# Kernel optimization log

Hardware: AMD Instinct MI355X
Metric: run time of the kernel (lower is better)

Reference implementation:

```python
import jax, jax.numpy as jnp
from jax import lax
import numpy as np

EPS = 1e-5  # BatchNorm eps


def setup_inputs() -> dict:
    key = jax.random.key(0)
    ks = jax.random.split(key, 4)
    T, B, C = 256, 128, 1024
    L, H, NCLS = 6, 1024, 1000
    x = jax.random.normal(ks[0], (T, B, C), dtype=jnp.float32)
    W = jax.random.normal(ks[1], (L, C, H), dtype=jnp.float32) * (1.0 / np.sqrt(C))
    b = jnp.zeros((L, H), dtype=jnp.float32)
    gamma = jnp.ones((L, H), dtype=jnp.float32)
    beta = jnp.zeros((L, H), dtype=jnp.float32)
    u = jax.random.uniform(ks[2], (L, H), dtype=jnp.float32)  # recurrent weights in (0, U_bound~1)
    Wc = jax.random.normal(ks[3], (H, NCLS), dtype=jnp.float32) * (1.0 / np.sqrt(H))
    bc = jnp.zeros((NCLS,), dtype=jnp.float32)
    return {"x": x, "W": W, "b": b, "gamma": gamma, "beta": beta, "u": u, "Wc": Wc, "bc": bc}


def _layer(h, Wl, bl, gl, betal, ul):
    # per-timestep dense projection: [T,B,Cin] @ [Cin,H]
    z = jnp.einsum('tbi,ih->tbh', h, Wl) + bl
    # BN over (time, batch) per channel (bn_before, training-mode batch stats)
    mean = jnp.mean(z, axis=(0, 1))
    var = jnp.var(z, axis=(0, 1))
    z = (z - mean) * (gl / jnp.sqrt(var + EPS)) + betal
    # IndRNN diagonal recurrence: h_t = relu(z_t + u * h_{t-1}), h_0 = 0
    T, B, H = z.shape
    def step(hprev, zt):
        hnew = jax.nn.relu(zt + ul * hprev)
        return hnew, hnew
    _, hs = lax.scan(step, jnp.zeros((B, H), dtype=z.dtype), z)
    return hs


def reference(x, W, b, gamma, beta, u, Wc, bc):
    h = x
    for l in range(W.shape[0]):
        h = _layer(h, W[l], b[l], gamma[l], beta[l], u[l])
    # classifier on last timestep
    return h[-1] @ Wc + bc
```

## Files before the change

kernel.cpp:

```cpp
#include <hip/hip_runtime.h>
#include <hip/hip_bf16.h>

#define T_DIM 256
#define B_DIM 128
#define C_DIM 1024
#define H_DIM 1024
#define L_DIM 6
#define NC_DIM 1000
#define M_DIM (T_DIM * B_DIM)
#define BH_DIM (B_DIM * H_DIM)

typedef __attribute__((ext_vector_type(8))) short bf16x8;
typedef __attribute__((ext_vector_type(4))) float f32x4;

__device__ __forceinline__ float bf2f(unsigned short u) {
  union { unsigned int i; float f; } v; v.i = ((unsigned int)u) << 16; return v.f;
}
__device__ __forceinline__ unsigned short f2bf(float f) {
  union { float f; unsigned int i; } v; v.f = f;
  unsigned int r = v.i + 0x7fffu + ((v.i >> 16) & 1u);
  return (unsigned short)(r >> 16);
}

__device__ __forceinline__ void gload_lds16(const void* g, void* l) {
  __builtin_amdgcn_global_load_lds(
      (const __attribute__((address_space(1))) unsigned int*)g,
      (__attribute__((address_space(3))) unsigned int*)l, 16, 0, 0);
}

__global__ __launch_bounds__(256) void f32_to_bf16_kernel(
    const float* __restrict__ in, unsigned short* __restrict__ out, int n4) {
  int stride = gridDim.x * blockDim.x;
  for (int i = blockIdx.x * blockDim.x + threadIdx.x; i < n4; i += stride) {
    float4 v = ((const float4*)in)[i];
    ushort4 o;
    o.x = f2bf(v.x); o.y = f2bf(v.y); o.z = f2bf(v.z); o.w = f2bf(v.w);
    ((ushort4*)out)[i] = o;
  }
}

__global__ __launch_bounds__(256) void wtrans_kernel(
    const float* __restrict__ W, unsigned short* __restrict__ Wt) {
  __shared__ float tile[32][33];
  int l = blockIdx.z;
  const float* Wl = W + (size_t)l * C_DIM * H_DIM;
  unsigned short* Wtl = Wt + (size_t)l * C_DIM * H_DIM;
  int h0 = blockIdx.x * 32, c0 = blockIdx.y * 32;
  int tx = threadIdx.x, ty = threadIdx.y;
#pragma unroll
  for (int i = 0; i < 32; i += 8)
    tile[ty + i][tx] = Wl[(size_t)(c0 + ty + i) * H_DIM + h0 + tx];
  __syncthreads();
#pragma unroll
  for (int i = 0; i < 32; i += 8)
    Wtl[(size_t)(h0 + ty + i) * C_DIM + c0 + tx] = f2bf(tile[tx][ty + i]);
}

#define NT 32

__global__ __launch_bounds__(512, 2) void gemm_kernel(
    const unsigned short* __restrict__ A, const unsigned short* __restrict__ Bt,
    unsigned short* __restrict__ Z, float* __restrict__ psum, float* __restrict__ psqs) {
  extern __shared__ char lds[];
  int bid = blockIdx.x;
  int swz = (bid & 7) * 64 + (bid >> 3);
  int tm = swz >> 2, tn = swz & 3;
  int tid = threadIdx.x;
  int wv = tid >> 6, ln = tid & 63;
  int wm = wv >> 2, wn = wv & 3;

  const char* Apanel = (const char*)A + (size_t)tm * 256 * 2048;
  const char* Bpanel = (const char*)Bt + (size_t)tn * 256 * 2048;

  int p0 = wv * 1024 + ln * 16;
  int l0 = p0 ^ (((p0 >> 7) & 3) << 4);
  size_t ro0 = (size_t)(p0 >> 6) * 2048 + (l0 & 63);
  size_t ro1 = (size_t)(128 + (p0 >> 6)) * 2048 + (l0 & 63);
  int sdst = wv * 1024;

  auto stage = [&](int t) {
    char* base = lds + ((t & 3) * 32768);
    int kb = t * 64;
    gload_lds16(Apanel + ro0 + kb, base + sdst);
    gload_lds16(Apanel + ro1 + kb, base + 8192 + sdst);
    gload_lds16(Bpanel + ro0 + kb, base + 16384 + sdst);
    gload_lds16(Bpanel + ro1 + kb, base + 16384 + 8192 + sdst);
  };

  int frow = ln & 15;
  int fchunk = ((ln >> 4) ^ (frow >> 1)) & 3;
  int floff = frow * 64 + (fchunk << 4);

  f32x4 acc[8][4];
  f32x4 zero = {0.f, 0.f, 0.f, 0.f};
#pragma unroll
  for (int m = 0; m < 8; ++m)
#pragma unroll
    for (int n = 0; n < 4; ++n) acc[m][n] = zero;

  bf16x8 bX[4], aP[4], aQ[4];
  auto readB_to = [&](int t, bf16x8* d) {
    const char* Bb = lds + ((t & 3) * 32768) + 16384 + wn * 4096;
#pragma unroll
    for (int n = 0; n < 4; ++n) d[n] = *(const bf16x8*)(Bb + n * 1024 + floff);
  };
  auto readA_to = [&](int t, int mq, bf16x8* d) {
    const char* Ab = lds + ((t & 3) * 32768) + wm * 8192 + mq * 4096;
#pragma unroll
    for (int i = 0; i < 4; ++i) d[i] = *(const bf16x8*)(Ab + i * 1024 + floff);
  };

  stage(0); stage(1); stage(2);
  asm volatile("s_waitcnt vmcnt(4)" ::: "memory");
  __builtin_amdgcn_s_barrier();
  readB_to(0, bX); readA_to(0, 0, aP);

  for (int t = 0; t < NT; ++t) {
    readA_to(t, 1, aQ);
    if (t <= NT - 4) stage(t + 3);
    __builtin_amdgcn_s_setprio(1);
#pragma unroll
    for (int i = 0; i < 4; ++i)
#pragma unroll
      for (int n = 0; n < 4; ++n)
        acc[i][n] = __builtin_amdgcn_mfma_f32_16x16x32_bf16(aP[i], bX[n], acc[i][n], 0, 0, 0);
    __builtin_amdgcn_s_setprio(0);
    __builtin_amdgcn_s_setprio(1);
#pragma unroll
    for (int i = 0; i < 4; ++i)
#pragma unroll
      for (int n = 0; n < 4; ++n)
        acc[4 + i][n] = __builtin_amdgcn_mfma_f32_16x16x32_bf16(aQ[i], bX[n], acc[4 + i][n], 0, 0, 0);
    __builtin_amdgcn_s_setprio(0);
    if (t < NT - 1) {
      readB_to(t + 1, bX); readA_to(t + 1, 0, aP);
      if (t <= NT - 4) { asm volatile("s_waitcnt vmcnt(4)" ::: "memory"); }
      else             { asm volatile("s_waitcnt vmcnt(0)" ::: "memory"); }
      __builtin_amdgcn_s_barrier();
    }
  }

  float s[4], q[4];
#pragma unroll
  for (int n = 0; n < 4; ++n) {
    float sv = 0.f, qv = 0.f;
#pragma unroll
    for (int m = 0; m < 8; ++m)
#pragma unroll
      for (int r = 0; r < 4; ++r) {
        float v = acc[m][n][r];
        sv += v; qv += v * v;
      }
    s[n] = sv; q[n] = qv;
  }
#pragma unroll
  for (int n = 0; n < 4; ++n) {
    s[n] += __shfl_xor(s[n], 16); s[n] += __shfl_xor(s[n], 32);
    q[n] += __shfl_xor(q[n], 16); q[n] += __shfl_xor(q[n], 32);
  }
  float* red = (float*)lds;
  if (ln < 16) {
#pragma unroll
    for (int n = 0; n < 4; ++n) {
      red[wm * 256 + wn * 64 + n * 16 + ln] = s[n];
      red[512 + wm * 256 + wn * 64 + n * 16 + ln] = q[n];
    }
  }
  __syncthreads();
  if (tid < 256) {
    psum[(size_t)tm * H_DIM + tn * 256 + tid] = red[tid] + red[256 + tid];
  } else {
    int c = tid - 256;
    psqs[(size_t)tm * H_DIM + tn * 256 + c] = red[512 + c] + red[768 + c];
  }
  int r0 = tm * 256 + wm * 128 + ((ln >> 4) << 2);
  int c0 = tn * 256 + wn * 64 + (ln & 15);
#pragma unroll
  for (int m = 0; m < 8; ++m)
#pragma unroll
    for (int n = 0; n < 4; ++n) {
      unsigned short* zp = Z + (size_t)(r0 + m * 16) * H_DIM + c0 + n * 16;
#pragma unroll
      for (int r = 0; r < 4; ++r) zp[(size_t)r * H_DIM] = f2bf(acc[m][n][r]);
    }
}

__global__ __launch_bounds__(256) void bn_finalize_kernel(
    const float* __restrict__ psum, const float* __restrict__ psqs,
    const float* __restrict__ gamma, const float* __restrict__ beta,
    float* __restrict__ ss) {
  int c = blockIdx.x * blockDim.x + threadIdx.x;
  float s = 0.f, q = 0.f;
  for (int i = 0; i < 128; ++i) {
    s += psum[(size_t)i * H_DIM + c];
    q += psqs[(size_t)i * H_DIM + c];
  }
  const float invN = 1.0f / (float)M_DIM;
  float mean = s * invN;
  float var = q * invN - mean * mean;
  float sc = gamma[c] * rsqrtf(var + 1e-5f);
  ss[c] = sc;
  ss[H_DIM + c] = beta[c] - mean * sc;
}

__global__ __launch_bounds__(256) void bn_recur_kernel(
    const unsigned short* __restrict__ Z, const float* __restrict__ ss,
    const float* __restrict__ u, unsigned short* __restrict__ Hout) {
  int i = blockIdx.x * 256 + threadIdx.x;
  int h = i & (H_DIM - 1);
  float sc = ss[h], sh = ss[H_DIM + h], uu = u[h];
  float hv = 0.f;
  const unsigned short* Zt = Z + i;
  unsigned short* Ht = Hout + i;

  unsigned short za[32], zb[32];
#pragma unroll
  for (int j = 0; j < 32; ++j) za[j] = Zt[(size_t)j * BH_DIM];

#pragma unroll
  for (int blk = 0; blk < 4; ++blk) {
    int tA = blk * 64;
#pragma unroll
    for (int j = 0; j < 32; ++j) zb[j] = Zt[(size_t)(tA + 32 + j) * BH_DIM];
#pragma unroll
    for (int j = 0; j < 32; ++j) {
      float z = fmaf(bf2f(za[j]), sc, sh);
      hv = fmaxf(fmaf(uu, hv, z), 0.f);
      Ht[(size_t)(tA + j) * BH_DIM] = f2bf(hv);
    }
    if (blk < 3) {
#pragma unroll
      for (int j = 0; j < 32; ++j) za[j] = Zt[(size_t)(tA + 64 + j) * BH_DIM];
    }
#pragma unroll
    for (int j = 0; j < 32; ++j) {
      float z = fmaf(bf2f(zb[j]), sc, sh);
      hv = fmaxf(fmaf(uu, hv, z), 0.f);
      Ht[(size_t)(tA + 32 + j) * BH_DIM] = f2bf(hv);
    }
  }
}

__global__ __launch_bounds__(256) void classifier_kernel(
    const unsigned short* __restrict__ hlast, const float* __restrict__ Wc,
    const float* __restrict__ bc, float* __restrict__ out) {
  __shared__ float hs[H_DIM];
  int b = blockIdx.y;
  int n = blockIdx.x * 256 + threadIdx.x;
  for (int k = threadIdx.x; k < H_DIM; k += 256)
    hs[k] = bf2f(hlast[(size_t)b * H_DIM + k]);
  __syncthreads();
  if (n < NC_DIM) {
    float acc = bc[n];
#pragma unroll 8
    for (int k = 0; k < H_DIM; ++k)
      acc = fmaf(hs[k], Wc[(size_t)k * NC_DIM + n], acc);
    out[(size_t)b * NC_DIM + n] = acc;
  }
}

extern "C" void kernel_launch(void* const* d_in, const int* in_sizes, int n_in,
                              void* d_out, int out_size, void* d_ws, size_t ws_size,
                              hipStream_t stream) {
  const float* x     = (const float*)d_in[0];
  const float* W     = (const float*)d_in[1];
  const float* gamma = (const float*)d_in[3];
  const float* beta  = (const float*)d_in[4];
  const float* u     = (const float*)d_in[5];
  const float* Wc    = (const float*)d_in[6];
  const float* bc    = (const float*)d_in[7];
  float* out = (float*)d_out;

  const size_t CH = (size_t)C_DIM * H_DIM;
  const size_t MH = (size_t)M_DIM * H_DIM;
  char* p = (char*)d_ws;
  unsigned short* Wt = (unsigned short*)p; p += L_DIM * CH * sizeof(unsigned short);
  unsigned short* Ha = (unsigned short*)p; p += MH * sizeof(unsigned short);
  unsigned short* Hb = (unsigned short*)p; p += MH * sizeof(unsigned short);
  unsigned short* Z  = (unsigned short*)p; p += MH * sizeof(unsigned short);
  float* psum = (float*)p; p += 128 * H_DIM * sizeof(float);
  float* psqs = (float*)p; p += 128 * H_DIM * sizeof(float);
  float* ss   = (float*)p; p += 2 * H_DIM * sizeof(float);

  f32_to_bf16_kernel<<<2048, 256, 0, stream>>>(x, Ha, (int)(MH / 4));
  wtrans_kernel<<<dim3(H_DIM / 32, C_DIM / 32, L_DIM), dim3(32, 8), 0, stream>>>(W, Wt);

  unsigned short* cur = Ha;
  unsigned short* nxt = Hb;
  for (int l = 0; l < L_DIM; ++l) {
    gemm_kernel<<<(M_DIM / 256) * (H_DIM / 256), 512, 131072, stream>>>(
        cur, Wt + (size_t)l * CH, Z, psum, psqs);
    bn_finalize_kernel<<<4, 256, 0, stream>>>(psum, psqs, gamma + (size_t)l * H_DIM,
                                              beta + (size_t)l * H_DIM, ss);
    bn_recur_kernel<<<BH_DIM / 256, 256, 0, stream>>>(Z, ss, u + (size_t)l * H_DIM, nxt);
    unsigned short* tmp = cur; cur = nxt; nxt = tmp;
  }
  classifier_kernel<<<dim3(4, B_DIM), 256, 0, stream>>>(
      cur + (size_t)(T_DIM - 1) * BH_DIM, Wc, bc, out);
}
```

Before: 753.0 us.

## Make GEMM blocks process two M-tiles and fold BN finalize into recurrence

Each GEMM workgroup now computes two consecutive 256-row tiles. The grid is cut to 256 blocks, so every block is resident in a single wave on the device. The next tile's first K stages are prefetched while the previous tile's epilogue runs, and the reduction scratch moves to the unused fourth LDS buffer. The separate bn_finalize launch is removed: each recurrence thread re-reduces the 128 partial sums for its channel itself. This trades one launch and one tail effect for redundant partial-sum reads across the 128 batch threads that share a channel.

```diff
diff --git a/kernel.cpp b/kernel.cpp
--- a/kernel.cpp
+++ b/kernel.cpp
@@ -63,13 +63,15 @@
     unsigned short* __restrict__ Z, float* __restrict__ psum, float* __restrict__ psqs) {
   extern __shared__ char lds[];
   int bid = blockIdx.x;
-  int swz = (bid & 7) * 64 + (bid >> 3);
-  int tm = swz >> 2, tn = swz & 3;
+  int swz = (bid & 7) * 32 + (bid >> 3);
+  int tm0 = (swz >> 2) * 2;
+  int tn = swz & 3;
   int tid = threadIdx.x;
   int wv = tid >> 6, ln = tid & 63;
   int wm = wv >> 2, wn = wv & 3;
 
-  const char* Apanel = (const char*)A + (size_t)tm * 256 * 2048;
+  const char* Ap0 = (const char*)A + (size_t)tm0 * 256 * 2048;
+  const char* Ap1 = Ap0 + (size_t)256 * 2048;
   const char* Bpanel = (const char*)Bt + (size_t)tn * 256 * 2048;
 
   int p0 = wv * 1024 + ln * 16;
@@ -78,11 +80,11 @@
   size_t ro1 = (size_t)(128 + (p0 >> 6)) * 2048 + (l0 & 63);
   int sdst = wv * 1024;
 
-  auto stage = [&](int t) {
+  auto stage = [&](const char* Ap, int t) {
     char* base = lds + ((t & 3) * 32768);
     int kb = t * 64;
-    gload_lds16(Apanel + ro0 + kb, base + sdst);
-    gload_lds16(Apanel + ro1 + kb, base + 8192 + sdst);
+    gload_lds16(Ap + ro0 + kb, base + sdst);
+    gload_lds16(Ap + ro1 + kb, base + 8192 + sdst);
     gload_lds16(Bpanel + ro0 + kb, base + 16384 + sdst);
     gload_lds16(Bpanel + ro1 + kb, base + 16384 + 8192 + sdst);
   };
@@ -92,11 +94,6 @@
   int floff = frow * 64 + (fchunk << 4);
 
   f32x4 acc[8][4];
-  f32x4 zero = {0.f, 0.f, 0.f, 0.f};
-#pragma unroll
-  for (int m = 0; m < 8; ++m)
-#pragma unroll
-    for (int n = 0; n < 4; ++n) acc[m][n] = zero;
 
   bf16x8 bX[4], aP[4], aQ[4];
   auto readB_to = [&](int t, bf16x8* d) {
@@ -110,105 +107,120 @@
     for (int i = 0; i < 4; ++i) d[i] = *(const bf16x8*)(Ab + i * 1024 + floff);
   };
 
-  stage(0); stage(1); stage(2);
+  auto kloop = [&](const char* Ap) {
+    f32x4 zero = {0.f, 0.f, 0.f, 0.f};
+#pragma unroll
+    for (int m = 0; m < 8; ++m)
+#pragma unroll
+      for (int n = 0; n < 4; ++n) acc[m][n] = zero;
+    readB_to(0, bX); readA_to(0, 0, aP);
+    for (int t = 0; t < NT; ++t) {
+      readA_to(t, 1, aQ);
+      if (t <= NT - 4) stage(Ap, t + 3);
+      __builtin_amdgcn_s_setprio(1);
+#pragma unroll
+      for (int i = 0; i < 4; ++i)
+#pragma unroll
+        for (int n = 0; n < 4; ++n)
+          acc[i][n] = __builtin_amdgcn_mfma_f32_16x16x32_bf16(aP[i], bX[n], acc[i][n], 0, 0, 0);
+      __builtin_amdgcn_s_setprio(0);
+      __builtin_amdgcn_s_setprio(1);
+#pragma unroll
+      for (int i = 0; i < 4; ++i)
+#pragma unroll
+        for (int n = 0; n < 4; ++n)
+          acc[4 + i][n] = __builtin_amdgcn_mfma_f32_16x16x32_bf16(aQ[i], bX[n], acc[4 + i][n], 0, 0, 0);
+      __builtin_amdgcn_s_setprio(0);
+      if (t < NT - 1) {
+        readB_to(t + 1, bX); readA_to(t + 1, 0, aP);
+        if (t <= NT - 4) { asm volatile("s_waitcnt vmcnt(4)" ::: "memory"); }
+        else             { asm volatile("s_waitcnt vmcnt(0)" ::: "memory"); }
+        __builtin_amdgcn_s_barrier();
+      }
+    }
+  };
+
+  float* red = (float*)(lds + 3 * 32768);
+  auto epilogue = [&](int tm) {
+    float s[4], q[4];
+#pragma unroll
+    for (int n = 0; n < 4; ++n) {
+      float sv = 0.f, qv = 0.f;
+#pragma unroll
+      for (int m = 0; m < 8; ++m)
+#pragma unroll
+        for (int r = 0; r < 4; ++r) {
+          float v = acc[m][n][r];
+          sv += v; qv += v * v;
+        }
+      s[n] = sv; q[n] = qv;
+    }
+#pragma unroll
+    for (int n = 0; n < 4; ++n) {
+      s[n] += __shfl_xor(s[n], 16); s[n] += __shfl_xor(s[n], 32);
+      q[n] += __shfl_xor(q[n], 16); q[n] += __shfl_xor(q[n], 32);
+    }
+    if (ln < 16) {
+#pragma unroll
+      for (int n = 0; n < 4; ++n) {
+        red[wm * 256 + wn * 64 + n * 16 + ln] = s[n];
+        red[512 + wm * 256 + wn * 64 + n * 16 + ln] = q[n];
+      }
+    }
+    __syncthreads();
+    if (tid < 256) {
+      psum[(size_t)tm * H_DIM + tn * 256 + tid] = red[tid] + red[256 + tid];
+    } else {
+      int c = tid - 256;
+      psqs[(size_t)tm * H_DIM + tn * 256 + c] = red[512 + c] + red[768 + c];
+    }
+    __syncthreads();
+    int r0 = tm * 256 + wm * 128 + ((ln >> 4) << 2);
+    int c0 = tn * 256 + wn * 64 + (ln & 15);
+#pragma unroll
+    for (int m = 0; m < 8; ++m)
+#pragma unroll
+      for (int n = 0; n < 4; ++n) {
+        unsigned short* zp = Z + (size_t)(r0 + m * 16) * H_DIM + c0 + n * 16;
+#pragma unroll
+        for (int r = 0; r < 4; ++r) zp[(size_t)r * H_DIM] = f2bf(acc[m][n][r]);
+      }
+  };
+
+  stage(Ap0, 0); stage(Ap0, 1); stage(Ap0, 2);
   asm volatile("s_waitcnt vmcnt(4)" ::: "memory");
   __builtin_amdgcn_s_barrier();
-  readB_to(0, bX); readA_to(0, 0, aP);
-
-  for (int t = 0; t < NT; ++t) {
-    readA_to(t, 1, aQ);
-    if (t <= NT - 4) stage(t + 3);
-    __builtin_amdgcn_s_setprio(1);
-#pragma unroll
-    for (int i = 0; i < 4; ++i)
-#pragma unroll
-      for (int n = 0; n < 4; ++n)
-        acc[i][n] = __builtin_amdgcn_mfma_f32_16x16x32_bf16(aP[i], bX[n], acc[i][n], 0, 0, 0);
-    __builtin_amdgcn_s_setprio(0);
-    __builtin_amdgcn_s_setprio(1);
-#pragma unroll
-    for (int i = 0; i < 4; ++i)
-#pragma unroll
-      for (int n = 0; n < 4; ++n)
-        acc[4 + i][n] = __builtin_amdgcn_mfma_f32_16x16x32_bf16(aQ[i], bX[n], acc[4 + i][n], 0, 0, 0);
-    __builtin_amdgcn_s_setprio(0);
-    if (t < NT - 1) {
-      readB_to(t + 1, bX); readA_to(t + 1, 0, aP);
-      if (t <= NT - 4) { asm volatile("s_waitcnt vmcnt(4)" ::: "memory"); }
-      else             { asm volatile("s_waitcnt vmcnt(0)" ::: "memory"); }
-      __builtin_amdgcn_s_barrier();
-    }
-  }
-
-  float s[4], q[4];
-#pragma unroll
-  for (int n = 0; n < 4; ++n) {
-    float sv = 0.f, qv = 0.f;
-#pragma unroll
-    for (int m = 0; m < 8; ++m)
-#pragma unroll
-      for (int r = 0; r < 4; ++r) {
-        float v = acc[m][n][r];
-        sv += v; qv += v * v;
-      }
-    s[n] = sv; q[n] = qv;
-  }
-#pragma unroll
-  for (int n = 0; n < 4; ++n) {
-    s[n] += __shfl_xor(s[n], 16); s[n] += __shfl_xor(s[n], 32);
-    q[n] += __shfl_xor(q[n], 16); q[n] += __shfl_xor(q[n], 32);
-  }
-  float* red = (float*)lds;
-  if (ln < 16) {
-#pragma unroll
-    for (int n = 0; n < 4; ++n) {
-      red[wm * 256 + wn * 64 + n * 16 + ln] = s[n];
-      red[512 + wm * 256 + wn * 64 + n * 16 + ln] = q[n];
-    }
-  }
-  __syncthreads();
-  if (tid < 256) {
-    psum[(size_t)tm * H_DIM + tn * 256 + tid] = red[tid] + red[256 + tid];
-  } else {
-    int c = tid - 256;
-    psqs[(size_t)tm * H_DIM + tn * 256 + c] = red[512 + c] + red[768 + c];
-  }
-  int r0 = tm * 256 + wm * 128 + ((ln >> 4) << 2);
-  int c0 = tn * 256 + wn * 64 + (ln & 15);
-#pragma unroll
-  for (int m = 0; m < 8; ++m)
-#pragma unroll
-    for (int n = 0; n < 4; ++n) {
-      unsigned short* zp = Z + (size_t)(r0 + m * 16) * H_DIM + c0 + n * 16;
-#pragma unroll
-      for (int r = 0; r < 4; ++r) zp[(size_t)r * H_DIM] = f2bf(acc[m][n][r]);
-    }
-}
-
-__global__ __launch_bounds__(256) void bn_finalize_kernel(
-    const float* __restrict__ psum, const float* __restrict__ psqs,
-    const float* __restrict__ gamma, const float* __restrict__ beta,
-    float* __restrict__ ss) {
-  int c = blockIdx.x * blockDim.x + threadIdx.x;
+  kloop(Ap0);
+  __builtin_amdgcn_s_barrier();
+  stage(Ap1, 0); stage(Ap1, 1); stage(Ap1, 2);
+  epilogue(tm0);
+  asm volatile("s_waitcnt vmcnt(4)" ::: "memory");
+  __builtin_amdgcn_s_barrier();
+  kloop(Ap1);
+  __builtin_amdgcn_s_barrier();
+  epilogue(tm0 + 1);
+}
+
+__global__ __launch_bounds__(256) void bn_recur_kernel(
+    const unsigned short* __restrict__ Z, const float* __restrict__ psum,
+    const float* __restrict__ psqs, const float* __restrict__ gamma,
+    const float* __restrict__ beta, const float* __restrict__ u,
+    unsigned short* __restrict__ Hout) {
+  int i = blockIdx.x * 256 + threadIdx.x;
+  int h = i & (H_DIM - 1);
   float s = 0.f, q = 0.f;
-  for (int i = 0; i < 128; ++i) {
-    s += psum[(size_t)i * H_DIM + c];
-    q += psqs[(size_t)i * H_DIM + c];
+#pragma unroll 8
+  for (int j = 0; j < 128; ++j) {
+    s += psum[(size_t)j * H_DIM + h];
+    q += psqs[(size_t)j * H_DIM + h];
   }
   const float invN = 1.0f / (float)M_DIM;
   float mean = s * invN;
   float var = q * invN - mean * mean;
-  float sc = gamma[c] * rsqrtf(var + 1e-5f);
-  ss[c] = sc;
-  ss[H_DIM + c] = beta[c] - mean * sc;
-}
-
-__global__ __launch_bounds__(256) void bn_recur_kernel(
-    const unsigned short* __restrict__ Z, const float* __restrict__ ss,
-    const float* __restrict__ u, unsigned short* __restrict__ Hout) {
-  int i = blockIdx.x * 256 + threadIdx.x;
-  int h = i & (H_DIM - 1);
-  float sc = ss[h], sh = ss[H_DIM + h], uu = u[h];
+  float sc = gamma[h] * rsqrtf(var + 1e-5f);
+  float sh = beta[h] - mean * sc;
+  float uu = u[h];
+
   float hv = 0.f;
   const unsigned short* Zt = Z + i;
   unsigned short* Ht = Hout + i;
@@ -280,7 +292,6 @@
   unsigned short* Z  = (unsigned short*)p; p += MH * sizeof(unsigned short);
   float* psum = (float*)p; p += 128 * H_DIM * sizeof(float);
   float* psqs = (float*)p; p += 128 * H_DIM * sizeof(float);
-  float* ss   = (float*)p; p += 2 * H_DIM * sizeof(float);
 
   f32_to_bf16_kernel<<<2048, 256, 0, stream>>>(x, Ha, (int)(MH / 4));
   wtrans_kernel<<<dim3(H_DIM / 32, C_DIM / 32, L_DIM), dim3(32, 8), 0, stream>>>(W, Wt);
@@ -288,11 +299,10 @@
   unsigned short* cur = Ha;
   unsigned short* nxt = Hb;
   for (int l = 0; l < L_DIM; ++l) {
-    gemm_kernel<<<(M_DIM / 256) * (H_DIM / 256), 512, 131072, stream>>>(
-        cur, Wt + (size_t)l * CH, Z, psum, psqs);
-    bn_finalize_kernel<<<4, 256, 0, stream>>>(psum, psqs, gamma + (size_t)l * H_DIM,
-                                              beta + (size_t)l * H_DIM, ss);
-    bn_recur_kernel<<<BH_DIM / 256, 256, 0, stream>>>(Z, ss, u + (size_t)l * H_DIM, nxt);
+    gemm_kernel<<<256, 512, 131072, stream>>>(cur, Wt + (size_t)l * CH, Z, psum, psqs);
+    bn_recur_kernel<<<BH_DIM / 256, 256, 0, stream>>>(
+        Z, psum, psqs, gamma + (size_t)l * H_DIM, beta + (size_t)l * H_DIM,
+        u + (size_t)l * H_DIM, nxt);
     unsigned short* tmp = cur; cur = nxt; nxt = tmp;
   }
   classifier_kernel<<<dim3(4, B_DIM), 256, 0, stream>>>(
```

Result: no change. 754.2 us (+0.2%).
